# Optimization experiments

Measured on AMD Instinct MI355X. Metric: run time of the kernel, lower is better.

Reference implementation:

```python
import jax, jax.numpy as jnp
import numpy as np

DIM = 256
NH = 8
KA = 3
DR = 4
CR = DIM // DR            # 64 reduced dim
CPH = CR // NH            # 8 channels per head
SCALE = (DIM // NH) ** -0.5  # head_dim uses full dim, per original code


def _unfold_kernel():
    # fixed identity depthwise kernel: out channel c*KA*KA+i picks window offset i of channel c
    eye = jnp.eye(KA * KA, dtype=jnp.float32).reshape(KA * KA, 1, KA, KA)
    return jnp.tile(eye, (CPH, 1, 1, 1))  # (KA*KA*CPH, 1, KA, KA)


def _dwconv(x, w, b):
    # x: (N, CPH, H, W), w: (KA*KA*CPH, 1, KA, KA), groups=CPH, 'same' zero padding
    y = jax.lax.conv_general_dilated(
        x, w, window_strides=(1, 1), padding=[(KA // 2, KA // 2)] * 2,
        dimension_numbers=("NCHW", "OIHW", "NCHW"), feature_group_count=CPH)
    return y + b[None, :, None, None]


def setup_inputs() -> dict:
    key = jax.random.key(0)
    ks = jax.random.split(key, 8)
    B, L = 16, 4096
    x = jax.random.normal(ks[0], (B, L, DIM), dtype=jnp.float32)
    qkv_w = jax.random.normal(ks[1], (3 * CR, DIM), dtype=jnp.float32) * 0.02
    qkv_b = jnp.zeros((3 * CR,), dtype=jnp.float32)
    dep_conv_b = jax.random.normal(ks[2], (KA * KA * CPH,), dtype=jnp.float32) * 0.02
    dep_conv1_w = jax.random.normal(ks[3], (KA * KA * CPH, 1, KA, KA), dtype=jnp.float32) * 0.02
    dep_conv1_b = jnp.zeros((KA * KA * CPH,), dtype=jnp.float32)
    rpb_table = jax.random.normal(ks[4], (1, NH, 1, KA * KA, 1, 1), dtype=jnp.float32) * 0.02
    proj_w = jax.random.normal(ks[5], (DIM, CR), dtype=jnp.float32) * 0.02
    proj_b = jnp.zeros((DIM,), dtype=jnp.float32)
    return {
        "x": x, "H22": 64, "W22": 64,
        "relative_pos_index": jax.random.randint(ks[6], (9, 9), 0, 9),
        "relative_coords_table": jax.random.normal(ks[7], (9, 2), dtype=jnp.float32),
        "qkv_w": qkv_w, "qkv_b": qkv_b,
        "dep_conv_b": dep_conv_b, "dep_conv1_w": dep_conv1_w, "dep_conv1_b": dep_conv1_b,
        "rpb_table": rpb_table, "proj_w": proj_w, "proj_b": proj_b,
    }


def reference(x, H22, W22, relative_pos_index, relative_coords_table,
              qkv_w, qkv_b, dep_conv_b, dep_conv1_w, dep_conv1_b,
              rpb_table, proj_w, proj_b):
    B1, L1, C1 = x.shape
    H = int(np.sqrt(L1)); W = H
    # faithful to original: reshape (B,L,C)->(B,C,H,W) then move channels last
    xhw = x.reshape(B1, C1, H, W).transpose(0, 2, 3, 1)       # (B,H,W,C)
    qkv = xhw @ qkv_w.T + qkv_b                               # (B,H,W,3*CR)
    f = qkv.transpose(0, 3, 1, 2).reshape(B1 * NH, 3 * CPH, H, W)
    q = (f[:, :CPH] * SCALE).reshape(B1, NH, CPH, 1, H, W)
    kk = f[:, CPH:2 * CPH]                                    # (B*NH, CPH, H, W)
    vv = f[:, 2 * CPH:]
    w0 = _unfold_kernel()
    k = _dwconv(kk, w0, dep_conv_b) + _dwconv(kk, dep_conv1_w, dep_conv1_b)
    v = _dwconv(vv, w0, dep_conv_b) + _dwconv(vv, dep_conv1_w, dep_conv1_b)
    k = k.reshape(B1, NH, CPH, KA * KA, H, W) + rpb_table     # rpb bias on k
    v = v.reshape(B1, NH, CPH, KA * KA, H, W)
    attn = jax.nn.softmax((q * k).sum(2, keepdims=True), axis=3)  # (B,NH,1,ka*ka,H,W)
    out = (attn * v).sum(3).reshape(B1, CR, H, W).transpose(0, 2, 3, 1)  # (B,H,W,CR)
    out = out @ proj_w.T + proj_b                              # (B,H,W,C1)
    return out.transpose(0, 3, 1, 2).reshape(B1, L1, C1)
```

## Files before the change

### kernel.cpp

```cpp
#include <hip/hip_runtime.h>

#define BB 16
#define HW 4096
#define DIMC 256
#define NHEAD 8
#define CPH 8
#define NQKV 192
#define SCALE 0.17677669529663687f

typedef __attribute__((ext_vector_type(8))) short bf16x8;
typedef __attribute__((ext_vector_type(4))) float f32x4;

__device__ inline unsigned short f2b(float f) {
  union { float f; unsigned int u; } x; x.f = f;
  unsigned int r = x.u + 0x7FFFu + ((x.u >> 16) & 1u);
  return (unsigned short)(r >> 16);
}
__device__ inline float b2f(unsigned short u) {
  union { unsigned int u; float f; } x; x.u = ((unsigned int)u) << 16;
  return x.f;
}
__device__ inline void async_copy16(const void* g, void* l) {
  __builtin_amdgcn_global_load_lds((const __attribute__((address_space(1))) void*)g,
                                   (__attribute__((address_space(3))) void*)l, 16, 0, 0);
}

__global__ __launch_bounds__(256) void cast_xT(const float* __restrict__ x,
                                               unsigned short* __restrict__ xT) {
  __shared__ float Xs[64][69];
  const int b = blockIdx.z;
  const int k0 = blockIdx.y * 64;
  const int s0 = blockIdx.x * 64;
  const int tid = threadIdx.x;
  const float* xb = x + (size_t)b * (DIMC * HW);
#pragma unroll
  for (int i = 0; i < 4; ++i) {
    int idx = tid + i * 256;
    int kr = idx >> 4, f = idx & 15;
    float4 v = *(const float4*)&xb[(size_t)(k0 + kr) * HW + s0 + f * 4];
    Xs[kr][f * 4 + 0] = v.x; Xs[kr][f * 4 + 1] = v.y;
    Xs[kr][f * 4 + 2] = v.z; Xs[kr][f * 4 + 3] = v.w;
  }
  __syncthreads();
  unsigned short* ob = xT + (size_t)b * (HW * DIMC);
#pragma unroll
  for (int i = 0; i < 2; ++i) {
    int slot = tid + i * 256;
    int sr = slot >> 3, g8 = slot & 7;
    unsigned short pk[8];
#pragma unroll
    for (int j = 0; j < 8; ++j) pk[j] = f2b(Xs[g8 * 8 + j][sr]);
    *(uint4*)&ob[(size_t)(s0 + sr) * DIMC + k0 + g8 * 8] = *(uint4*)pk;
  }
}

__global__ __launch_bounds__(256) void cast_qw(const float* __restrict__ qw,
                                               unsigned short* __restrict__ qwf) {
  int t = blockIdx.x * 256 + threadIdx.x;
  int lane = t & 63;
  int cell = t >> 6;
  int m = lane & 15, g = lane >> 4;
  int band = cell >> 3, c32 = cell & 7;
  int j = band * 16 + m;
  int k = c32 * 32 + g * 8;
  unsigned short pk[8];
#pragma unroll
  for (int i = 0; i < 8; ++i) pk[i] = f2b(qw[j * 256 + k + i]);
  *(uint4*)&qwf[(size_t)t * 8] = *(uint4*)pk;
}

__global__ __launch_bounds__(256) void cast_pw(const float* __restrict__ pw,
                                               unsigned short* __restrict__ pwf) {
  int t = blockIdx.x * 256 + threadIdx.x;
  int lane = t & 63;
  int cell = t >> 6;
  int m = lane & 15, g = lane >> 4;
  int band = cell >> 1, c32 = cell & 1;
  int d = band * 16 + m;
  int j = c32 * 32 + g * 8;
  unsigned short pk[8];
#pragma unroll
  for (int i = 0; i < 8; ++i) pk[i] = f2b(pw[d * 64 + j + i]);
  *(uint4*)&pwf[(size_t)t * 8] = *(uint4*)pk;
}

__global__ __launch_bounds__(256) void qkv_mfma(const unsigned short* __restrict__ xT,
                                                const unsigned short* __restrict__ qwf,
                                                const float* __restrict__ qb,
                                                unsigned short* __restrict__ qkvt) {
  __shared__ unsigned short Bs[128 * 256];
  const int b = blockIdx.y;
  const int s_blk = blockIdx.x * 128;
  const int tid = threadIdx.x;
  const int wave = tid >> 6, lane = tid & 63;

  {
    const int row_in = lane >> 5, cst = lane & 31;
#pragma unroll
    for (int ii = 0; ii < 16; ++ii) {
      int i = wave * 16 + ii;
      int s_row = 2 * i + row_in;
      int mem_chunk = (cst & 24) | ((cst ^ s_row) & 7);
      const unsigned short* src =
          xT + ((size_t)b * HW + s_blk + s_row) * DIMC + mem_chunk * 8;
      async_copy16(src, (char*)Bs + i * 1024);
    }
  }
  __syncthreads();

  f32x4 acc[3][8];
#pragma unroll
  for (int t = 0; t < 3; ++t)
#pragma unroll
    for (int st = 0; st < 8; ++st) acc[t][st] = (f32x4){0.f, 0.f, 0.f, 0.f};

  const int n = lane & 15, g = lane >> 4;
#pragma unroll
  for (int c32 = 0; c32 < 8; ++c32) {
    bf16x8 af[3];
#pragma unroll
    for (int t = 0; t < 3; ++t) {
      int band = wave * 3 + t;
      af[t] = *(const bf16x8*)(qwf + ((size_t)(band * 8 + c32) * 64 + lane) * 8);
    }
#pragma unroll
    for (int st = 0; st < 8; ++st) {
      int s_row = st * 16 + n;
      int mc = c32 * 4 + g;
      int stc = (mc & 24) | ((mc ^ s_row) & 7);
      bf16x8 bf = *(const bf16x8*)&Bs[s_row * 256 + stc * 8];
#pragma unroll
      for (int t = 0; t < 3; ++t)
        acc[t][st] = __builtin_amdgcn_mfma_f32_16x16x32_bf16(af[t], bf, acc[t][st], 0, 0, 0);
    }
  }

  unsigned short* ob = qkvt + (size_t)b * (NQKV * HW);
#pragma unroll
  for (int t = 0; t < 3; ++t) {
    int j0 = (wave * 3 + t) * 16 + g * 4;
#pragma unroll
    for (int st = 0; st < 8; ++st) {
      int s = s_blk + st * 16 + n;
#pragma unroll
      for (int r = 0; r < 4; ++r) {
        float v = acc[t][st][r] + qb[j0 + r];
        ob[(size_t)(j0 + r) * HW + s] = f2b(v);
      }
    }
  }
}

__global__ __launch_bounds__(512, 2) void attn_kernel(const unsigned short* __restrict__ qkvt,
                                                      const float* __restrict__ dcb,
                                                      const float* __restrict__ w1,
                                                      const float* __restrict__ dc1b,
                                                      const float* __restrict__ rpb,
                                                      unsigned short* __restrict__ aoT) {
  __shared__ float hal[16][10][20];
  __shared__ float plog[8][9][128];
  __shared__ __align__(16) float wA[8][84];
  __shared__ float dsum[72];
  __shared__ float rpbn[9];
  __shared__ unsigned short ot[128][8];

  const int bn = blockIdx.x;
  const int tile = blockIdx.y;
  const int b = bn >> 3, n = bn & 7;
  const int h0 = (tile >> 2) * 8, w0 = (tile & 3) * 16;
  const int tid = threadIdx.x;
  const int c = tid >> 6, lane = tid & 63;
  const int ly = lane >> 4, lx = lane & 15;
  const int s0 = (h0 + ly) * 64 + (w0 + lx);
  const int s1 = s0 + 256;
  const unsigned short* fb = qkvt + ((size_t)b * NQKV + n * 24) * HW;

  for (int e = tid; e < 2880; e += 512) {
    int cb = e / 180;
    int rem = e - cb * 180;
    int y = rem / 18, xx = rem - y * 18;
    int gy = h0 - 1 + y, gx = w0 - 1 + xx;
    float v = 0.f;
    if ((unsigned)gy < 64u && (unsigned)gx < 64u)
      v = b2f(fb[(size_t)(8 + cb) * HW + gy * 64 + gx]);
    hal[cb][y][xx] = v;
  }
  for (int e = tid; e < 648; e += 512) {
    int cc = e / 81;
    wA[cc][e - cc * 81] = w1[e];
  }
  if (tid < 72) dsum[tid] = dcb[tid] + dc1b[tid];
  else if (tid >= 128 && tid < 137) rpbn[tid - 128] = rpb[n * 9 + (tid - 128)];

  float qc0 = SCALE * b2f(fb[(size_t)c * HW + s0]);
  float qc1 = SCALE * b2f(fb[(size_t)c * HW + s1]);
  __syncthreads();

  float Af[81];
#pragma unroll
  for (int i = 0; i < 20; ++i) {
    float4 v = *(const float4*)&wA[c][i * 4];
    Af[i * 4 + 0] = v.x; Af[i * 4 + 1] = v.y;
    Af[i * 4 + 2] = v.z; Af[i * 4 + 3] = v.w;
  }
  Af[80] = wA[c][80];
#pragma unroll
  for (int p = 0; p < 9; ++p) Af[p * 9 + p] += 1.f;

  {
    float2 t[9];
#pragma unroll
    for (int dy = 0; dy < 3; ++dy)
#pragma unroll
      for (int dx = 0; dx < 3; ++dx)
        t[dy * 3 + dx] = make_float2(hal[c][ly + dy][lx + dx],
                                     hal[c][ly + 4 + dy][lx + dx]);
#pragma unroll
    for (int p = 0; p < 9; ++p) {
      float base = dsum[c * 9 + p] + rpbn[p];
      float kx = base, ky = base;
#pragma unroll
      for (int rs = 0; rs < 9; ++rs) {
        kx = fmaf(Af[p * 9 + rs], t[rs].x, kx);
        ky = fmaf(Af[p * 9 + rs], t[rs].y, ky);
      }
      plog[c][p][lane] = qc0 * kx;
      plog[c][p][lane + 64] = qc1 * ky;
    }
  }
  __syncthreads();

  for (int it = tid; it < 1152; it += 512) {
    int p = it >> 7, px = it & 127;
    float sum = plog[0][p][px] + plog[1][p][px] + plog[2][p][px] + plog[3][p][px] +
                plog[4][p][px] + plog[5][p][px] + plog[6][p][px] + plog[7][p][px];
    plog[0][p][px] = sum;
  }
  __syncthreads();

  float ax[9], ay[9];
  {
    float mx = -1e30f, my = -1e30f;
#pragma unroll
    for (int p = 0; p < 9; ++p) {
      ax[p] = plog[0][p][lane];
      ay[p] = plog[0][p][lane + 64];
      mx = fmaxf(mx, ax[p]); my = fmaxf(my, ay[p]);
    }
    float dx = 0.f, dy = 0.f;
#pragma unroll
    for (int p = 0; p < 9; ++p) {
      ax[p] = __expf(ax[p] - mx); dx += ax[p];
      ay[p] = __expf(ay[p] - my); dy += ay[p];
    }
    float ix = 1.f / dx, iy = 1.f / dy;
#pragma unroll
    for (int p = 0; p < 9; ++p) { ax[p] *= ix; ay[p] *= iy; }
  }

  {
    float2 t[9];
#pragma unroll
    for (int dy = 0; dy < 3; ++dy)
#pragma unroll
      for (int dx = 0; dx < 3; ++dx)
        t[dy * 3 + dx] = make_float2(hal[8 + c][ly + dy][lx + dx],
                                     hal[8 + c][ly + 4 + dy][lx + dx]);
    float ocx = 0.f, ocy = 0.f;
#pragma unroll
    for (int p = 0; p < 9; ++p) {
      float base = dsum[c * 9 + p];
      float vx = base, vy = base;
#pragma unroll
      for (int rs = 0; rs < 9; ++rs) {
        vx = fmaf(Af[p * 9 + rs], t[rs].x, vx);
        vy = fmaf(Af[p * 9 + rs], t[rs].y, vy);
      }
      ocx = fmaf(ax[p], vx, ocx);
      ocy = fmaf(ay[p], vy, ocy);
    }
    ot[lane][c] = f2b(ocx);
    ot[lane + 64][c] = f2b(ocy);
  }
  __syncthreads();

  if (c < 2) {
    int p = c * 64 + lane;
    uint4 val = *(const uint4*)&ot[p][0];
    int sp = (h0 + (p >> 4)) * 64 + w0 + (p & 15);
    *(uint4*)&aoT[((size_t)b * HW + sp) * 64 + n * 8] = val;
  }
}

__global__ __launch_bounds__(256) void proj_mfma(const unsigned short* __restrict__ aoT,
                                                 const unsigned short* __restrict__ pwf,
                                                 const float* __restrict__ pb,
                                                 float* __restrict__ out) {
  __shared__ unsigned short Bs[128 * 64];
  const int b = blockIdx.y;
  const int s_blk = blockIdx.x * 128;
  const int tid = threadIdx.x;
  const int wave = tid >> 6, lane = tid & 63;

  {
    const int slot = lane & 7, rsub = lane >> 3;
#pragma unroll
    for (int ii = 0; ii < 4; ++ii) {
      int i = wave * 4 + ii;
      int row = 8 * i + rsub;
      int mem_chunk = slot ^ rsub;
      const unsigned short* src =
          aoT + ((size_t)b * HW + s_blk + row) * 64 + mem_chunk * 8;
      async_copy16(src, (char*)Bs + i * 1024);
    }
  }
  __syncthreads();

  f32x4 acc[4][8];
#pragma unroll
  for (int t = 0; t < 4; ++t)
#pragma unroll
    for (int st = 0; st < 8; ++st) acc[t][st] = (f32x4){0.f, 0.f, 0.f, 0.f};

  const int n = lane & 15, g = lane >> 4;
#pragma unroll
  for (int c32 = 0; c32 < 2; ++c32) {
    bf16x8 af[4];
#pragma unroll
    for (int t = 0; t < 4; ++t) {
      int band = wave * 4 + t;
      af[t] = *(const bf16x8*)(pwf + ((size_t)(band * 2 + c32) * 64 + lane) * 8);
    }
#pragma unroll
    for (int st = 0; st < 8; ++st) {
      int s_row = st * 16 + n;
      int mc = c32 * 4 + g;
      int stc = mc ^ (s_row & 7);
      bf16x8 bf = *(const bf16x8*)&Bs[s_row * 64 + stc * 8];
#pragma unroll
      for (int t = 0; t < 4; ++t)
        acc[t][st] = __builtin_amdgcn_mfma_f32_16x16x32_bf16(af[t], bf, acc[t][st], 0, 0, 0);
    }
  }

  float bias[4][4];
#pragma unroll
  for (int t = 0; t < 4; ++t)
#pragma unroll
    for (int r = 0; r < 4; ++r) bias[t][r] = pb[(wave * 4 + t) * 16 + g * 4 + r];

  float* ob = out + ((size_t)b << 20);
#pragma unroll
  for (int t = 0; t < 4; ++t) {
    int d0 = (wave * 4 + t) * 16 + g * 4;
#pragma unroll
    for (int st = 0; st < 8; ++st) {
      int s = s_blk + st * 16 + n;
#pragma unroll
      for (int r = 0; r < 4; ++r)
        ob[(size_t)(d0 + r) * HW + s] = acc[t][st][r] + bias[t][r];
    }
  }
}

extern "C" void kernel_launch(void* const* d_in, const int* in_sizes, int n_in,
                              void* d_out, int out_size, void* d_ws, size_t ws_size,
                              hipStream_t stream) {
  (void)in_sizes; (void)n_in; (void)out_size; (void)ws_size;
  const float* x    = (const float*)d_in[0];
  const float* qw   = (const float*)d_in[5];
  const float* qb   = (const float*)d_in[6];
  const float* dcb  = (const float*)d_in[7];
  const float* w1   = (const float*)d_in[8];
  const float* dc1b = (const float*)d_in[9];
  const float* rpb  = (const float*)d_in[10];
  const float* pw   = (const float*)d_in[11];
  const float* pb   = (const float*)d_in[12];

  unsigned short* qkvt = (unsigned short*)d_ws;
  unsigned short* qwf  = (unsigned short*)((char*)d_ws + 25165824);
  unsigned short* aoT  = (unsigned short*)((char*)d_ws + 25165824);
  unsigned short* xT   = (unsigned short*)((char*)d_ws + 33554432);
  unsigned short* pwf  = (unsigned short*)((char*)d_ws + 33554432);

  cast_qw<<<24, 256, 0, stream>>>(qw, qwf);
  cast_xT<<<dim3(64, 4, BB), 256, 0, stream>>>(x, xT);
  qkv_mfma<<<dim3(32, BB), 256, 0, stream>>>(xT, qwf, qb, qkvt);
  cast_pw<<<8, 256, 0, stream>>>(pw, pwf);
  attn_kernel<<<dim3(BB * NHEAD, 32), 512, 0, stream>>>(qkvt, dcb, w1, dc1b, rpb, aoT);
  proj_mfma<<<dim3(32, BB), 256, 0, stream>>>(aoT, pwf, pb, (float*)d_out);
}
```

Before: 226.5 us.

## Precompute conv weights/biases once, shrink attention LDS, atomic head-sum reduction

```diff
diff --git a/kernel.cpp b/kernel.cpp
--- a/kernel.cpp
+++ b/kernel.cpp
@@ -55,7 +55,29 @@
 }
 
 __global__ __launch_bounds__(256) void cast_qw(const float* __restrict__ qw,
-                                               unsigned short* __restrict__ qwf) {
+                                               unsigned short* __restrict__ qwf,
+                                               const float* __restrict__ dcb,
+                                               const float* __restrict__ w1,
+                                               const float* __restrict__ dc1b,
+                                               const float* __restrict__ rpb,
+                                               float* __restrict__ prep) {
+  if (blockIdx.x == 24) {
+    for (int e = threadIdx.x; e < 1056; e += 256) {
+      float v = 0.f;
+      if (e < 864) {
+        int cp = e / 12, rs = e - cp * 12;
+        if (rs < 9) v = w1[cp * 9 + rs] + ((cp % 9) == rs ? 1.f : 0.f);
+      } else if (e < 960) {
+        int i = e - 864; int c = i / 12, p = i - c * 12;
+        if (p < 9) v = dcb[c * 9 + p] + dc1b[c * 9 + p];
+      } else {
+        int i = e - 960; int n = i / 12, p = i - n * 12;
+        if (p < 9) v = rpb[n * 9 + p];
+      }
+      prep[e] = v;
+    }
+    return;
+  }
   int t = blockIdx.x * 256 + threadIdx.x;
   int lane = t & 63;
   int cell = t >> 6;
@@ -151,17 +173,11 @@
   }
 }
 
-__global__ __launch_bounds__(512, 2) void attn_kernel(const unsigned short* __restrict__ qkvt,
-                                                      const float* __restrict__ dcb,
-                                                      const float* __restrict__ w1,
-                                                      const float* __restrict__ dc1b,
-                                                      const float* __restrict__ rpb,
+__global__ __launch_bounds__(512, 4) void attn_kernel(const unsigned short* __restrict__ qkvt,
+                                                      const float* __restrict__ prep,
                                                       unsigned short* __restrict__ aoT) {
-  __shared__ float hal[16][10][20];
-  __shared__ float plog[8][9][128];
-  __shared__ __align__(16) float wA[8][84];
-  __shared__ float dsum[72];
-  __shared__ float rpbn[9];
+  __shared__ float2 hal2[16][6][20];
+  __shared__ float plog[9][128];
   __shared__ unsigned short ot[128][8];
 
   const int bn = blockIdx.x;
@@ -175,6 +191,8 @@
   const int s1 = s0 + 256;
   const unsigned short* fb = qkvt + ((size_t)b * NQKV + n * 24) * HW;
 
+  for (int e = tid; e < 1152; e += 512) ((float*)plog)[e] = 0.f;
+
   for (int e = tid; e < 2880; e += 512) {
     int cb = e / 180;
     int rem = e - cb * 180;
@@ -183,58 +201,52 @@
     float v = 0.f;
     if ((unsigned)gy < 64u && (unsigned)gx < 64u)
       v = b2f(fb[(size_t)(8 + cb) * HW + gy * 64 + gx]);
-    hal[cb][y][xx] = v;
-  }
-  for (int e = tid; e < 648; e += 512) {
-    int cc = e / 81;
-    wA[cc][e - cc * 81] = w1[e];
-  }
-  if (tid < 72) dsum[tid] = dcb[tid] + dc1b[tid];
-  else if (tid >= 128 && tid < 137) rpbn[tid - 128] = rpb[n * 9 + (tid - 128)];
+    if (y < 6) hal2[cb][y][xx].x = v;
+    if (y >= 4) hal2[cb][y - 4][xx].y = v;
+  }
+
+  float Af[81];
+  {
+    const float* ap = prep + c * 108;
+#pragma unroll
+    for (int p = 0; p < 9; ++p) {
+      float4 a0 = *(const float4*)(ap + p * 12);
+      float4 a1 = *(const float4*)(ap + p * 12 + 4);
+      Af[p * 9 + 0] = a0.x; Af[p * 9 + 1] = a0.y; Af[p * 9 + 2] = a0.z; Af[p * 9 + 3] = a0.w;
+      Af[p * 9 + 4] = a1.x; Af[p * 9 + 5] = a1.y; Af[p * 9 + 6] = a1.z; Af[p * 9 + 7] = a1.w;
+      Af[p * 9 + 8] = ap[p * 12 + 8];
+    }
+  }
+  float Kb[9], Vb[9];
+  {
+    const float* vp = prep + 864 + c * 12;
+    const float* rp = prep + 960 + n * 12;
+#pragma unroll
+    for (int p = 0; p < 9; ++p) { float d = vp[p]; Vb[p] = d; Kb[p] = d + rp[p]; }
+  }
 
   float qc0 = SCALE * b2f(fb[(size_t)c * HW + s0]);
   float qc1 = SCALE * b2f(fb[(size_t)c * HW + s1]);
   __syncthreads();
 
-  float Af[81];
-#pragma unroll
-  for (int i = 0; i < 20; ++i) {
-    float4 v = *(const float4*)&wA[c][i * 4];
-    Af[i * 4 + 0] = v.x; Af[i * 4 + 1] = v.y;
-    Af[i * 4 + 2] = v.z; Af[i * 4 + 3] = v.w;
-  }
-  Af[80] = wA[c][80];
-#pragma unroll
-  for (int p = 0; p < 9; ++p) Af[p * 9 + p] += 1.f;
-
   {
     float2 t[9];
 #pragma unroll
     for (int dy = 0; dy < 3; ++dy)
 #pragma unroll
       for (int dx = 0; dx < 3; ++dx)
-        t[dy * 3 + dx] = make_float2(hal[c][ly + dy][lx + dx],
-                                     hal[c][ly + 4 + dy][lx + dx]);
+        t[dy * 3 + dx] = hal2[c][ly + dy][lx + dx];
 #pragma unroll
     for (int p = 0; p < 9; ++p) {
-      float base = dsum[c * 9 + p] + rpbn[p];
-      float kx = base, ky = base;
+      float kx = Kb[p], ky = Kb[p];
 #pragma unroll
       for (int rs = 0; rs < 9; ++rs) {
         kx = fmaf(Af[p * 9 + rs], t[rs].x, kx);
         ky = fmaf(Af[p * 9 + rs], t[rs].y, ky);
       }
-      plog[c][p][lane] = qc0 * kx;
-      plog[c][p][lane + 64] = qc1 * ky;
-    }
-  }
-  __syncthreads();
-
-  for (int it = tid; it < 1152; it += 512) {
-    int p = it >> 7, px = it & 127;
-    float sum = plog[0][p][px] + plog[1][p][px] + plog[2][p][px] + plog[3][p][px] +
-                plog[4][p][px] + plog[5][p][px] + plog[6][p][px] + plog[7][p][px];
-    plog[0][p][px] = sum;
+      atomicAdd(&plog[p][lane], qc0 * kx);
+      atomicAdd(&plog[p][lane + 64], qc1 * ky);
+    }
   }
   __syncthreads();
 
@@ -243,8 +255,8 @@
     float mx = -1e30f, my = -1e30f;
 #pragma unroll
     for (int p = 0; p < 9; ++p) {
-      ax[p] = plog[0][p][lane];
-      ay[p] = plog[0][p][lane + 64];
+      ax[p] = plog[p][lane];
+      ay[p] = plog[p][lane + 64];
       mx = fmaxf(mx, ax[p]); my = fmaxf(my, ay[p]);
     }
     float dx = 0.f, dy = 0.f;
@@ -264,13 +276,11 @@
     for (int dy = 0; dy < 3; ++dy)
 #pragma unroll
       for (int dx = 0; dx < 3; ++dx)
-        t[dy * 3 + dx] = make_float2(hal[8 + c][ly + dy][lx + dx],
-                                     hal[8 + c][ly + 4 + dy][lx + dx]);
+        t[dy * 3 + dx] = hal2[8 + c][ly + dy][lx + dx];
     float ocx = 0.f, ocy = 0.f;
 #pragma unroll
     for (int p = 0; p < 9; ++p) {
-      float base = dsum[c * 9 + p];
-      float vx = base, vy = base;
+      float vx = Vb[p], vy = Vb[p];
 #pragma unroll
       for (int rs = 0; rs < 9; ++rs) {
         vx = fmaf(Af[p * 9 + rs], t[rs].x, vx);
@@ -382,11 +392,12 @@
   unsigned short* aoT  = (unsigned short*)((char*)d_ws + 25165824);
   unsigned short* xT   = (unsigned short*)((char*)d_ws + 33554432);
   unsigned short* pwf  = (unsigned short*)((char*)d_ws + 33554432);
-
-  cast_qw<<<24, 256, 0, stream>>>(qw, qwf);
+  float* prep          = (float*)d_out;
+
+  cast_qw<<<25, 256, 0, stream>>>(qw, qwf, dcb, w1, dc1b, rpb, prep);
   cast_xT<<<dim3(64, 4, BB), 256, 0, stream>>>(x, xT);
   qkv_mfma<<<dim3(32, BB), 256, 0, stream>>>(xT, qwf, qb, qkvt);
   cast_pw<<<8, 256, 0, stream>>>(pw, pwf);
-  attn_kernel<<<dim3(BB * NHEAD, 32), 512, 0, stream>>>(qkvt, dcb, w1, dc1b, rpb, aoT);
+  attn_kernel<<<dim3(BB * NHEAD, 32), 512, 0, stream>>>(qkvt, prep, aoT);
   proj_mfma<<<dim3(32, BB), 256, 0, stream>>>(aoT, pwf, pb, (float*)d_out);
 }
```

After: 403.9 us. 1.78x slower.
